# Kernel optimization log

Measured on AMD Instinct MI355X. Metric: run time of the kernel, lower is better.

Reference implementation:

```python
import jax, jax.numpy as jnp
import numpy as np
from jax import lax

K = 5          # kernel_size
OC = 8         # out_num_capsules
OD = 32        # out_dims


def setup_inputs() -> dict:
    key = jax.random.key(0)
    k1, k2, k3 = jax.random.split(key, 3)
    u = jax.random.normal(k1, (4, 4, 16, 128, 128), jnp.float32)            # [B, in_caps, in_dims, H, W]
    W = jax.random.normal(k2, (4, OC * OD, 16, K, K), jnp.float32) * 0.05    # per-capsule Conv2d weights (OIHW)
    bias = jax.random.normal(k3, (4, OC * OD), jnp.float32) * 0.05
    return {"u": u, "W": W, "bias": bias}


def _squash(p):
    # p: [..., out_dims]
    sq = jnp.sum(p * p, axis=-1, keepdims=True)
    return sq / (1.0 + sq) * p / jnp.sqrt(sq + 1e-9)


def reference(u, W, bias):
    B, ic, _, H, Wd = u.shape

    def conv_one(x, w, b):  # x:[B,in_dims,H,W] w:[OC*OD,in_dims,K,K]
        y = lax.conv_general_dilated(x, w, (1, 1), [(2, 2), (2, 2)],
                                     dimension_numbers=("NCHW", "OIHW", "NCHW"))
        return y + b[None, :, None, None]

    # per-capsule conv, vmapped over the in_capsule axis -> [B, ic, OC*OD, H, W]
    u_hat = jax.vmap(conv_one, in_axes=(1, 0, 0), out_axes=1)(u, W, bias)
    # -> [B, ic, H, W, OC, OD] (matches torch reshape + transpose_(1,3).transpose_(2,4))
    u_hat = u_hat.reshape(B, ic, OC, OD, H, Wd).transpose(0, 1, 4, 5, 2, 3)

    # Routing logits b start at zero. NOTE: in the source, the update `b_t_list_`
    # is a dead store (never assigned back), so b stays zero for all iterations
    # and every routing iteration produces the identical v; one effective pass.
    b_r = jnp.zeros((B, OC, H, Wd), u.dtype)
    # windowed max (torch max_pool2d pads with -inf; k=5, pad=2 == SAME)
    b_max = lax.reduce_window(b_r, -jnp.inf, lax.max, (1, 1, K, K), (1, 1, 1, 1), "SAME")
    b_max = jnp.max(b_max, axis=1, keepdims=True)                 # [B,1,H,W]
    c = jnp.exp(b_r - b_max)                                      # [B,OC,H,W]
    # conv2d_same with an all-ones (1, OC, K, K) kernel == channel-sum then SAME window-sum
    sum_c = lax.reduce_window(jnp.sum(c, axis=1, keepdims=True), 0.0, lax.add,
                              (1, 1, K, K), (1, 1, 1, 1), "SAME")  # [B,1,H,W]
    r = (c / sum_c).transpose(0, 2, 3, 1)[..., None]              # [B,H,W,OC,1]

    # r is identical for every input capsule (b==0), so fold the capsule sum
    p = jnp.sum(r[:, None] * u_hat, axis=1)                       # [B,H,W,OC,OD]
    v = _squash(p)
    # final v.transpose_(1,3).transpose_(2,4) -> [B, OC, OD, H, W]
    return v.transpose(0, 3, 4, 1, 2)
```

## Files before the change

### kernel.cpp

```cpp
#include <hip/hip_runtime.h>
#include <math.h>

typedef __attribute__((ext_vector_type(8))) __bf16 b16x8;
typedef __attribute__((ext_vector_type(4))) float f32x4;

__device__ __forceinline__ unsigned short f2bf(float x) {
    unsigned int v = __float_as_uint(x);
    v += 0x7fffu + ((v >> 16) & 1u);
    return (unsigned short)(v >> 16);
}

__device__ __forceinline__ float red16(float x) {
    int v;
    v = __builtin_amdgcn_update_dpp(0, __float_as_int(x), 0xB1, 0xF, 0xF, true);
    x += __int_as_float(v);
    v = __builtin_amdgcn_update_dpp(0, __float_as_int(x), 0x4E, 0xF, 0xF, true);
    x += __int_as_float(v);
    v = __builtin_amdgcn_update_dpp(0, __float_as_int(x), 0x141, 0xF, 0xF, true);
    x += __int_as_float(v);
    v = __builtin_amdgcn_update_dpp(0, __float_as_int(x), 0x140, 0xF, 0xF, true);
    x += __int_as_float(v);
    return x;
}

__global__ __launch_bounds__(256) void repack_w(
    const float* __restrict__ Wt, const float* __restrict__ bias,
    unsigned short* __restrict__ wsw, float* __restrict__ wsb) {
    int idx = blockIdx.x * 256 + threadIdx.x;
    if (idx < 409600) {
        int j    = idx & 7;
        int lane = (idx >> 3) & 63;
        int fr   = (idx >> 9) & 1;
        int wn   = (idx >> 10) & 7;
        int l    = idx >> 13;
        int kh   = l % 5;
        int ks   = (l / 5) & 1;
        int kw   = l / 10;
        int tap  = kh * 5 + kw;
        int col  = lane & 15;
        int cg   = lane >> 4;
        int o    = wn * 32 + fr * 16 + col;
        int cin  = ks * 32 + cg * 8 + j;
        int ic = cin >> 4, id = cin & 15;
        float w = Wt[((size_t)(ic * 256 + o) * 16 + id) * 25 + tap];
        wsw[idx] = f2bf(w);
    } else if (idx < 409856) {
        int o = idx - 409600;
        float s = 0.f;
        for (int ic = 0; ic < 4; ++ic) s += bias[ic * 256 + o];
        wsb[o] = s;
    }
}

__global__ __launch_bounds__(1024, 4) void caps_mfma(
    const float* __restrict__ u, const unsigned short* __restrict__ wsw,
    const float* __restrict__ wsb, float* __restrict__ out) {

    __shared__ __align__(16) unsigned short su_sh[25600];

    const int tid  = threadIdx.x;
    const int lane = tid & 63;
    const int wid  = tid >> 6;
    const int wm   = wid >> 3;
    const int wn   = wid & 7;
    const int col  = lane & 15;
    const int cg   = lane >> 4;
    const int ybase = wm * 8;

    const int bx  = blockIdx.x;
    const int b   = blockIdx.y;
    const int ty0 = (bx >> 3) * 16;
    const int tx0 = (bx & 7) * 16;

    f32x4 acc[8][2];
    #pragma unroll
    for (int f = 0; f < 8; ++f) {
        acc[f][0] = (f32x4)0.f;
        acc[f][1] = (f32x4)0.f;
    }

    auto stage_u = [&](int half) {
        const float* up = u + ((size_t)b * 64 + half * 32) * 16384;
        unsigned short* dstp = su_sh + half * 12800;
        #pragma unroll 1
        for (int i = tid; i < 12800; i += 1024) {
            int c = i / 400;
            int s = i - c * 400;
            int hy = s / 20, hx = s - hy * 20;
            int gy = ty0 - 2 + hy, gx = tx0 - 2 + hx;
            float v = 0.f;
            if ((unsigned)gy < 128u && (unsigned)gx < 128u)
                v = up[(size_t)c * 16384 + gy * 128 + gx];
            int cgp = (c >> 3) ^ ((hx >> 1) & 3);
            dstp[(hy * 20 + hx) * 32 + cgp * 8 + (c & 7)] = f2bf(v);
        }
    };

    const char* wp0 = ((const char*)wsw) + wn * 2048 + lane * 16;
    auto loadB = [&](int slot, b16x8* bf) {
        const char* p = wp0 + (size_t)slot * 16384;
        bf[0] = *reinterpret_cast<const b16x8*>(p);
        bf[1] = *reinterpret_cast<const b16x8*>(p + 1024);
    };

    b16x8 bfA[2], bfB[2];
    loadB(0, bfA);
    stage_u(0);
    stage_u(1);
    __syncthreads();

    #pragma unroll 1
    for (int g = 0; g < 5; ++g) {
        const int hx   = col + g;
        const int coff = hx * 32 + ((cg ^ ((hx >> 1) & 3)) * 8);
        const int l0   = g * 10;
        #pragma unroll
        for (int ks = 0; ks < 2; ++ks) {
            const unsigned short* apb =
                su_sh + ks * 12800 + ybase * 640 + coff;

            b16x8 aw[8];
            #pragma unroll
            for (int i = 0; i < 8; ++i)
                aw[i] = *reinterpret_cast<const b16x8*>(apb + i * 640);

            #pragma unroll
            for (int kh = 0; kh < 5; ++kh) {
                const int l  = l0 + ks * 5 + kh;
                const int ln = (l + 1 > 49) ? 49 : l + 1;
                b16x8* cur = ((ks * 5 + kh) & 1) ? bfB : bfA;
                b16x8* nxt = ((ks * 5 + kh) & 1) ? bfA : bfB;

                loadB(ln, nxt);

                __builtin_amdgcn_s_setprio(1);
                #pragma unroll
                for (int f = 0; f < 8; ++f) {
                    acc[f][0] = __builtin_amdgcn_mfma_f32_16x16x32_bf16(
                        aw[(kh + f) & 7], cur[0], acc[f][0], 0, 0, 0);
                    acc[f][1] = __builtin_amdgcn_mfma_f32_16x16x32_bf16(
                        aw[(kh + f) & 7], cur[1], acc[f][1], 0, 0, 0);
                }
                __builtin_amdgcn_s_setprio(0);

                if (kh < 4)
                    aw[kh & 7] = *reinterpret_cast<const b16x8*>(
                        apb + (kh + 8) * 640);
            }
        }
    }

    float bsv0 = wsb[wn * 32 + col];
    float bsv1 = wsb[wn * 32 + 16 + col];

    const int xg = lane >> 4;
    #pragma unroll
    for (int f = 0; f < 8; ++f) {
        int h = ty0 + ybase + f;
        int rows = min(h + 2, 127) - max(h - 2, 0) + 1;
        float o0[4], o1[4];
        #pragma unroll
        for (int r = 0; r < 4; ++r) {
            int w = tx0 + xg * 4 + r;
            int colsv = min(w + 2, 127) - max(w - 2, 0) + 1;
            float rs = 1.0f / (8.0f * (float)(rows * colsv));
            float p0 = (acc[f][0][r] + bsv0) * rs;
            float p1 = (acc[f][1][r] + bsv1) * rs;
            o0[r] = p0; o1[r] = p1;
            float sv = red16(p0 * p0 + p1 * p1);
            float scale = sv / ((1.0f + sv) * sqrtf(sv + 1e-9f));
            o0[r] *= scale; o1[r] *= scale;
        }
        size_t base = ((size_t)((b * 8 + wn) * 32) + col) * 16384
                      + (size_t)h * 128 + tx0 + xg * 4;
        float4 v0 = make_float4(o0[0], o0[1], o0[2], o0[3]);
        float4 v1 = make_float4(o1[0], o1[1], o1[2], o1[3]);
        *reinterpret_cast<float4*>(out + base) = v0;
        *reinterpret_cast<float4*>(out + base + (size_t)16 * 16384) = v1;
    }
}

extern "C" void kernel_launch(void* const* d_in, const int* in_sizes, int n_in,
                              void* d_out, int out_size, void* d_ws, size_t ws_size,
                              hipStream_t stream) {
    const float* u    = (const float*)d_in[0];
    const float* Wt   = (const float*)d_in[1];
    const float* bias = (const float*)d_in[2];
    unsigned short* wsw = (unsigned short*)d_ws;
    float* wsb = (float*)((char*)d_ws + 819200);

    repack_w<<<1601, 256, 0, stream>>>(Wt, bias, wsw, wsb);
    caps_mfma<<<dim3(64, 4), 1024, 0, stream>>>(u, wsw, wsb, (float*)d_out);
}
```

Before: 65.05 us.

## Halve spatial tile height to double block count and cut registers

Each block now covers an 8x16 output tile instead of 16x16, so the grid doubles to 512 blocks and each wave keeps 4 row-accumulators instead of 8. The shared-memory halo tile shrinks from 20x20 to 12x20 per channel, and the launch bound is raised to allow 8 waves per SIMD. The explicit weight-register double buffering and the sliding A-register window are removed, and A/B fragments are now loaded fresh on every tap. In exchange the halo overhead per output rises, weights are fetched twice as often overall, and load latency is no longer hidden by software prefetch.

```diff
diff --git a/kernel.cpp b/kernel.cpp
--- a/kernel.cpp
+++ b/kernel.cpp
@@ -52,100 +52,88 @@
     }
 }
 
-__global__ __launch_bounds__(1024, 4) void caps_mfma(
+__global__ __launch_bounds__(1024, 8) void caps_mfma(
     const float* __restrict__ u, const unsigned short* __restrict__ wsw,
     const float* __restrict__ wsb, float* __restrict__ out) {
 
-    __shared__ __align__(16) unsigned short su_sh[25600];
+    __shared__ __align__(16) unsigned short su_sh[15360];
 
     const int tid  = threadIdx.x;
     const int lane = tid & 63;
     const int wid  = tid >> 6;
-    const int wm   = wid >> 3;
+    const int pm   = wid >> 3;
     const int wn   = wid & 7;
     const int col  = lane & 15;
     const int cg   = lane >> 4;
-    const int ybase = wm * 8;
 
     const int bx  = blockIdx.x;
     const int b   = blockIdx.y;
-    const int ty0 = (bx >> 3) * 16;
+    const int ty0 = (bx >> 3) * 8;
     const int tx0 = (bx & 7) * 16;
 
-    f32x4 acc[8][2];
+    f32x4 acc[4][2];
     #pragma unroll
-    for (int f = 0; f < 8; ++f) {
+    for (int f = 0; f < 4; ++f) {
         acc[f][0] = (f32x4)0.f;
         acc[f][1] = (f32x4)0.f;
     }
 
-    auto stage_u = [&](int half) {
-        const float* up = u + ((size_t)b * 64 + half * 32) * 16384;
-        unsigned short* dstp = su_sh + half * 12800;
+    {
+        const float* up = u + (size_t)b * 64 * 16384;
         #pragma unroll 1
-        for (int i = tid; i < 12800; i += 1024) {
-            int c = i / 400;
-            int s = i - c * 400;
+        for (int i = tid; i < 15360; i += 1024) {
+            int c2 = i / 240;
+            int s  = i - c2 * 240;
             int hy = s / 20, hx = s - hy * 20;
             int gy = ty0 - 2 + hy, gx = tx0 - 2 + hx;
             float v = 0.f;
             if ((unsigned)gy < 128u && (unsigned)gx < 128u)
-                v = up[(size_t)c * 16384 + gy * 128 + gx];
+                v = up[(size_t)c2 * 16384 + gy * 128 + gx];
+            int c = c2 & 31;
             int cgp = (c >> 3) ^ ((hx >> 1) & 3);
-            dstp[(hy * 20 + hx) * 32 + cgp * 8 + (c & 7)] = f2bf(v);
+            su_sh[(c2 >> 5) * 7680 + (hy * 20 + hx) * 32 + cgp * 8 + (c & 7)]
+                = f2bf(v);
         }
-    };
-
-    const char* wp0 = ((const char*)wsw) + wn * 2048 + lane * 16;
-    auto loadB = [&](int slot, b16x8* bf) {
-        const char* p = wp0 + (size_t)slot * 16384;
-        bf[0] = *reinterpret_cast<const b16x8*>(p);
-        bf[1] = *reinterpret_cast<const b16x8*>(p + 1024);
-    };
-
-    b16x8 bfA[2], bfB[2];
-    loadB(0, bfA);
-    stage_u(0);
-    stage_u(1);
+    }
     __syncthreads();
 
-    #pragma unroll 1
+    const char* wp = ((const char*)wsw) + wn * 2048 + lane * 16;
+
+    #pragma unroll
     for (int g = 0; g < 5; ++g) {
         const int hx   = col + g;
         const int coff = hx * 32 + ((cg ^ ((hx >> 1) & 3)) * 8);
-        const int l0   = g * 10;
         #pragma unroll
         for (int ks = 0; ks < 2; ++ks) {
-            const unsigned short* apb =
-                su_sh + ks * 12800 + ybase * 640 + coff;
-
-            b16x8 aw[8];
-            #pragma unroll
-            for (int i = 0; i < 8; ++i)
-                aw[i] = *reinterpret_cast<const b16x8*>(apb + i * 640);
-
+            const unsigned short* apb = su_sh + ks * 7680 + pm * 4 * 640 + coff;
             #pragma unroll
             for (int kh = 0; kh < 5; ++kh) {
-                const int l  = l0 + ks * 5 + kh;
-                const int ln = (l + 1 > 49) ? 49 : l + 1;
-                b16x8* cur = ((ks * 5 + kh) & 1) ? bfB : bfA;
-                b16x8* nxt = ((ks * 5 + kh) & 1) ? bfA : bfB;
-
-                loadB(ln, nxt);
+                b16x8 bf0 = *reinterpret_cast<const b16x8*>(wp);
+                b16x8 bf1 = *reinterpret_cast<const b16x8*>(wp + 1024);
+                wp += 16384;
+                b16x8 a0 = *reinterpret_cast<const b16x8*>(apb + (kh    ) * 640);
+                b16x8 a1 = *reinterpret_cast<const b16x8*>(apb + (kh + 1) * 640);
+                b16x8 a2 = *reinterpret_cast<const b16x8*>(apb + (kh + 2) * 640);
+                b16x8 a3 = *reinterpret_cast<const b16x8*>(apb + (kh + 3) * 640);
 
                 __builtin_amdgcn_s_setprio(1);
-                #pragma unroll
-                for (int f = 0; f < 8; ++f) {
-                    acc[f][0] = __builtin_amdgcn_mfma_f32_16x16x32_bf16(
-                        aw[(kh + f) & 7], cur[0], acc[f][0], 0, 0, 0);
-                    acc[f][1] = __builtin_amdgcn_mfma_f32_16x16x32_bf16(
-                        aw[(kh + f) & 7], cur[1], acc[f][1], 0, 0, 0);
-                }
+                acc[0][0] = __builtin_amdgcn_mfma_f32_16x16x32_bf16(
+                    a0, bf0, acc[0][0], 0, 0, 0);
+                acc[0][1] = __builtin_amdgcn_mfma_f32_16x16x32_bf16(
+                    a0, bf1, acc[0][1], 0, 0, 0);
+                acc[1][0] = __builtin_amdgcn_mfma_f32_16x16x32_bf16(
+                    a1, bf0, acc[1][0], 0, 0, 0);
+                acc[1][1] = __builtin_amdgcn_mfma_f32_16x16x32_bf16(
+                    a1, bf1, acc[1][1], 0, 0, 0);
+                acc[2][0] = __builtin_amdgcn_mfma_f32_16x16x32_bf16(
+                    a2, bf0, acc[2][0], 0, 0, 0);
+                acc[2][1] = __builtin_amdgcn_mfma_f32_16x16x32_bf16(
+                    a2, bf1, acc[2][1], 0, 0, 0);
+                acc[3][0] = __builtin_amdgcn_mfma_f32_16x16x32_bf16(
+                    a3, bf0, acc[3][0], 0, 0, 0);
+                acc[3][1] = __builtin_amdgcn_mfma_f32_16x16x32_bf16(
+                    a3, bf1, acc[3][1], 0, 0, 0);
                 __builtin_amdgcn_s_setprio(0);
-
-                if (kh < 4)
-                    aw[kh & 7] = *reinterpret_cast<const b16x8*>(
-                        apb + (kh + 8) * 640);
             }
         }
     }
@@ -155,8 +143,8 @@
 
     const int xg = lane >> 4;
     #pragma unroll
-    for (int f = 0; f < 8; ++f) {
-        int h = ty0 + ybase + f;
+    for (int f = 0; f < 4; ++f) {
+        int h = ty0 + pm * 4 + f;
         int rows = min(h + 2, 127) - max(h - 2, 0) + 1;
         float o0[4], o1[4];
         #pragma unroll
@@ -190,5 +178,5 @@
     float* wsb = (float*)((char*)d_ws + 819200);
 
     repack_w<<<1601, 256, 0, stream>>>(Wt, bias, wsw, wsb);
-    caps_mfma<<<dim3(64, 4), 1024, 0, stream>>>(u, wsw, wsb, (float*)d_out);
+    caps_mfma<<<dim3(128, 4), 1024, 0, stream>>>(u, wsw, wsb, (float*)d_out);
 }
```

After: 80.70 us. +24.1%, slower.

## Swap MFMA operand roles, triple-buffer weight loads, and restructure squash epilogue

Applied to the files above, without the earlier changes.

Swaps the A/B operands of the MFMA so the accumulator's rows hold output dims instead of pixels. The squash norm then becomes mostly a per-thread sum plus two cross-lane shuffles instead of a 4-step DPP reduction for each element. Weight fragments are now prefetched two steps ahead with a triple buffer, and the tap loop is fully unrolled. The trade-off is in the output stores: each thread now writes scalar floats strided by channel planes instead of float4 rows, which coalesces across 16 lanes only. Full unrolling also raises register pressure under the 1024-thread launch bound.

```diff
diff --git a/kernel.cpp b/kernel.cpp
--- a/kernel.cpp
+++ b/kernel.cpp
@@ -8,19 +8,6 @@
     unsigned int v = __float_as_uint(x);
     v += 0x7fffu + ((v >> 16) & 1u);
     return (unsigned short)(v >> 16);
-}
-
-__device__ __forceinline__ float red16(float x) {
-    int v;
-    v = __builtin_amdgcn_update_dpp(0, __float_as_int(x), 0xB1, 0xF, 0xF, true);
-    x += __int_as_float(v);
-    v = __builtin_amdgcn_update_dpp(0, __float_as_int(x), 0x4E, 0xF, 0xF, true);
-    x += __int_as_float(v);
-    v = __builtin_amdgcn_update_dpp(0, __float_as_int(x), 0x141, 0xF, 0xF, true);
-    x += __int_as_float(v);
-    v = __builtin_amdgcn_update_dpp(0, __float_as_int(x), 0x140, 0xF, 0xF, true);
-    x += __int_as_float(v);
-    return x;
 }
 
 __global__ __launch_bounds__(256) void repack_w(
@@ -64,7 +51,7 @@
     const int wm   = wid >> 3;
     const int wn   = wid & 7;
     const int col  = lane & 15;
-    const int cg   = lane >> 4;
+    const int xg   = lane >> 4;
     const int ybase = wm * 8;
 
     const int bx  = blockIdx.x;
@@ -97,23 +84,25 @@
     };
 
     const char* wp0 = ((const char*)wsw) + wn * 2048 + lane * 16;
-    auto loadB = [&](int slot, b16x8* bf) {
-        const char* p = wp0 + (size_t)slot * 16384;
-        bf[0] = *reinterpret_cast<const b16x8*>(p);
-        bf[1] = *reinterpret_cast<const b16x8*>(p + 1024);
-    };
 
-    b16x8 bfA[2], bfB[2];
-    loadB(0, bfA);
+    b16x8 bf[3][2];
+    #define LOADB(SLOT, BUF)                                                   \
+        {                                                                      \
+            const char* p_ = wp0 + (size_t)((SLOT) > 49 ? 49 : (SLOT)) * 16384;\
+            bf[BUF][0] = *reinterpret_cast<const b16x8*>(p_);                  \
+            bf[BUF][1] = *reinterpret_cast<const b16x8*>(p_ + 1024);           \
+        }
+
+    LOADB(0, 0)
+    LOADB(1, 1)
     stage_u(0);
     stage_u(1);
     __syncthreads();
 
-    #pragma unroll 1
+    #pragma unroll
     for (int g = 0; g < 5; ++g) {
         const int hx   = col + g;
-        const int coff = hx * 32 + ((cg ^ ((hx >> 1) & 3)) * 8);
-        const int l0   = g * 10;
+        const int coff = hx * 32 + ((xg ^ ((hx >> 1) & 3)) * 8);
         #pragma unroll
         for (int ks = 0; ks < 2; ++ks) {
             const unsigned short* apb =
@@ -126,20 +115,17 @@
 
             #pragma unroll
             for (int kh = 0; kh < 5; ++kh) {
-                const int l  = l0 + ks * 5 + kh;
-                const int ln = (l + 1 > 49) ? 49 : l + 1;
-                b16x8* cur = ((ks * 5 + kh) & 1) ? bfB : bfA;
-                b16x8* nxt = ((ks * 5 + kh) & 1) ? bfA : bfB;
+                const int l = g * 10 + ks * 5 + kh;
 
-                loadB(ln, nxt);
+                LOADB(l + 2, (l + 2) % 3)
 
                 __builtin_amdgcn_s_setprio(1);
                 #pragma unroll
                 for (int f = 0; f < 8; ++f) {
                     acc[f][0] = __builtin_amdgcn_mfma_f32_16x16x32_bf16(
-                        aw[(kh + f) & 7], cur[0], acc[f][0], 0, 0, 0);
+                        bf[l % 3][0], aw[(kh + f) & 7], acc[f][0], 0, 0, 0);
                     acc[f][1] = __builtin_amdgcn_mfma_f32_16x16x32_bf16(
-                        aw[(kh + f) & 7], cur[1], acc[f][1], 0, 0, 0);
+                        bf[l % 3][1], aw[(kh + f) & 7], acc[f][1], 0, 0, 0);
                 }
                 __builtin_amdgcn_s_setprio(0);
 
@@ -149,34 +135,39 @@
             }
         }
     }
+    #undef LOADB
 
-    float bsv0 = wsb[wn * 32 + col];
-    float bsv1 = wsb[wn * 32 + 16 + col];
+    float4 bb0 = *reinterpret_cast<const float4*>(wsb + wn * 32 + xg * 4);
+    float4 bb1 = *reinterpret_cast<const float4*>(wsb + wn * 32 + 16 + xg * 4);
 
-    const int xg = lane >> 4;
+    const int x = tx0 + col;
+    const int colsv = min(x + 2, 127) - max(x - 2, 0) + 1;
+    float* pout = out + ((size_t)(b * 8 + wn) * 32 + xg * 4) * 16384 + x;
+
     #pragma unroll
     for (int f = 0; f < 8; ++f) {
         int h = ty0 + ybase + f;
         int rows = min(h + 2, 127) - max(h - 2, 0) + 1;
-        float o0[4], o1[4];
+        float rs = 1.0f / (8.0f * (float)(rows * colsv));
+        float p[8];
+        float sq = 0.f;
         #pragma unroll
         for (int r = 0; r < 4; ++r) {
-            int w = tx0 + xg * 4 + r;
-            int colsv = min(w + 2, 127) - max(w - 2, 0) + 1;
-            float rs = 1.0f / (8.0f * (float)(rows * colsv));
-            float p0 = (acc[f][0][r] + bsv0) * rs;
-            float p1 = (acc[f][1][r] + bsv1) * rs;
-            o0[r] = p0; o1[r] = p1;
-            float sv = red16(p0 * p0 + p1 * p1);
-            float scale = sv / ((1.0f + sv) * sqrtf(sv + 1e-9f));
-            o0[r] *= scale; o1[r] *= scale;
+            float v0 = (acc[f][0][r] + bb0[r]) * rs;
+            float v1 = (acc[f][1][r] + bb1[r]) * rs;
+            p[r] = v0; p[4 + r] = v1;
+            sq += v0 * v0;
+            sq += v1 * v1;
         }
-        size_t base = ((size_t)((b * 8 + wn) * 32) + col) * 16384
-                      + (size_t)h * 128 + tx0 + xg * 4;
-        float4 v0 = make_float4(o0[0], o0[1], o0[2], o0[3]);
-        float4 v1 = make_float4(o1[0], o1[1], o1[2], o1[3]);
-        *reinterpret_cast<float4*>(out + base) = v0;
-        *reinterpret_cast<float4*>(out + base + (size_t)16 * 16384) = v1;
+        sq += __shfl_xor(sq, 16);
+        sq += __shfl_xor(sq, 32);
+        float scale = sq / ((1.0f + sq) * sqrtf(sq + 1e-9f));
+        float* ph = pout + (size_t)h * 128;
+        #pragma unroll
+        for (int r = 0; r < 4; ++r) {
+            ph[(size_t)r * 16384]        = p[r] * scale;
+            ph[(size_t)(16 + r) * 16384] = p[4 + r] * scale;
+        }
     }
 }
 
```

Result: faster. 59.06 us (median of 2 runs) (-9.2%).
